# Kernel optimization log

Measured on AMD Instinct MI355X. Metric: run time of the kernel, lower is better.

Reference implementation:

```python
import jax, jax.numpy as jnp
import numpy as np

N_NODES = 100000
N_FEAT = 128
HID = 8
HEADS1 = 8
OUT2 = 32
NEG_SLOPE = 0.2


def gat_conv(x, W, a_src, a_dst, b, src, dst, n_nodes, concat):
    # x: [N, Fin], W: [Fin, H*C], a_src/a_dst: [H, C], b: [H*C] or [C]
    H, C = a_src.shape
    h = (x @ W).reshape(n_nodes, H, C)                      # [N, H, C]
    e_src = jnp.sum(h * a_src, axis=-1)                     # [N, H]
    e_dst = jnp.sum(h * a_dst, axis=-1)                     # [N, H]
    e = jax.nn.leaky_relu(e_src[src] + e_dst[dst], NEG_SLOPE)  # [E, H]
    m = jax.ops.segment_max(e, dst, num_segments=n_nodes)   # [N, H] (self-loops => no empty segment)
    ex = jnp.exp(e - m[dst])                                # [E, H]
    denom = jax.ops.segment_sum(ex, dst, num_segments=n_nodes)
    alpha = ex / denom[dst]                                 # [E, H]
    out = jax.ops.segment_sum(alpha[:, :, None] * h[src], dst, num_segments=n_nodes)  # [N, H, C]
    out = out.reshape(n_nodes, H * C) if concat else out.mean(axis=1)
    return out + b


def setup_inputs() -> dict:
    key = jax.random.key(0)
    ks = jax.random.split(key, 12)
    x = jax.random.normal(ks[0], (N_NODES, N_FEAT), dtype=jnp.float32)
    edge_index = jax.random.randint(ks[1], (2, 3200000), 0, N_NODES, dtype=jnp.int64)
    s1 = 1.0 / np.sqrt(N_FEAT)
    s2 = 1.0 / np.sqrt(HID * HEADS1)
    return {
        "x": x,
        "edge_index": edge_index,
        "W1": jax.random.normal(ks[2], (N_FEAT, HEADS1 * HID), dtype=jnp.float32) * s1,
        "a_src1": jax.random.normal(ks[3], (HEADS1, HID), dtype=jnp.float32) * s2,
        "a_dst1": jax.random.normal(ks[4], (HEADS1, HID), dtype=jnp.float32) * s2,
        "b1": jnp.zeros((HEADS1 * HID,), dtype=jnp.float32),
        "W2": jax.random.normal(ks[5], (HEADS1 * HID, OUT2), dtype=jnp.float32) * s2,
        "a_src2": jax.random.normal(ks[6], (1, OUT2), dtype=jnp.float32) * (1.0 / np.sqrt(OUT2)),
        "a_dst2": jax.random.normal(ks[7], (1, OUT2), dtype=jnp.float32) * (1.0 / np.sqrt(OUT2)),
        "b2": jnp.zeros((OUT2,), dtype=jnp.float32),
        "Wr": jax.random.normal(ks[8], (OUT2, 1), dtype=jnp.float32) * (1.0 / np.sqrt(OUT2)),
        "br": jnp.zeros((1,), dtype=jnp.float32),
    }


def reference(x, edge_index, W1, a_src1, a_dst1, b1, W2, a_src2, a_dst2, b2, Wr, br):
    n = x.shape[0]
    # PyG GATConv default add_self_loops=True
    loops = jnp.arange(n, dtype=edge_index.dtype)
    src = jnp.concatenate([edge_index[0], loops])
    dst = jnp.concatenate([edge_index[1], loops])
    h = gat_conv(x, W1, a_src1, a_dst1, b1, src, dst, n, concat=True)   # [N, 64]
    h = jax.nn.elu(h)
    h = gat_conv(h, W2, a_src2, a_dst2, b2, src, dst, n, concat=False)  # [N, 32]
    pooled = jnp.sum(h, axis=0, keepdims=True)                          # SumAggregation -> [1, 32]
    return pooled @ Wr + br                                             # [1, 1]
```

## Files before the change

### kernel.cpp

```cpp
#include <hip/hip_runtime.h>
#include <math.h>

#define NEG_SLOPE 0.2f
#define FIN 128
#define H1 8
#define F1 64
#define F2 32

#define SHIFT 5
#define BW 32
#define CAPL 2048
#define CAP_G 1408
#define NBMAX 4096

#define SB_SHIFT 11
#define NSBMAX 64
#define P_CHUNK 2048
#define BPS 35
#define SBCAP (BPS * P_CHUNK)

typedef unsigned short ushort_t;
typedef unsigned int uint_t;

#define LO16(u) __uint_as_float((u) << 16)
#define HI16(u) __uint_as_float((u) & 0xffff0000u)

#define FOLDQ4(x) { x += __shfl_xor(x, 16, 64); x += __shfl_xor(x, 32, 64); }
#define FOLD64(x) { x += __shfl_xor(x, 1, 64); x += __shfl_xor(x, 2, 64); x += __shfl_xor(x, 4, 64); \
                    x += __shfl_xor(x, 8, 64); x += __shfl_xor(x, 16, 64); x += __shfl_xor(x, 32, 64); }

static __device__ __forceinline__ ushort_t f2bf(float f) {
    uint_t u = __float_as_uint(f);
    u = (u + 0x7FFFu + ((u >> 16) & 1u)) >> 16;
    return (ushort_t)u;
}
static __device__ __forceinline__ uint_t packAB(float e) {
    return (uint_t)f2bf(__expf(e)) | ((uint_t)f2bf(__expf(NEG_SLOPE * e)) << 16);
}

__global__ void gemm1_kernel(const float* __restrict__ x, const float* __restrict__ W1,
                             const float* __restrict__ a_src, const float* __restrict__ a_dst,
                             ushort_t* __restrict__ h1, uint_t* __restrict__ sp,
                             float* __restrict__ ed, int N) {
    __shared__ float xs[16][FIN];
    int tid = threadIdx.x;
    int n0 = blockIdx.x * 16;
    for (int i = tid; i < 16 * FIN; i += 256) {
        int nn = n0 + (i >> 7);
        xs[i >> 7][i & 127] = (nn < N) ? x[(size_t)nn * FIN + (i & 127)] : 0.f;
    }
    __syncthreads();
    int wv = tid >> 6, j = tid & 63;
    int nb = wv << 2;
    float a0 = 0.f, a1 = 0.f, a2 = 0.f, a3 = 0.f;
#pragma unroll 2
    for (int k = 0; k < FIN; k += 4) {
        float w0 = W1[(k + 0) * F1 + j];
        float w1 = W1[(k + 1) * F1 + j];
        float w2 = W1[(k + 2) * F1 + j];
        float w3 = W1[(k + 3) * F1 + j];
        float4 x0 = *(const float4*)&xs[nb + 0][k];
        float4 x1 = *(const float4*)&xs[nb + 1][k];
        float4 x2 = *(const float4*)&xs[nb + 2][k];
        float4 x3 = *(const float4*)&xs[nb + 3][k];
        a0 = fmaf(x0.x, w0, fmaf(x0.y, w1, fmaf(x0.z, w2, fmaf(x0.w, w3, a0))));
        a1 = fmaf(x1.x, w0, fmaf(x1.y, w1, fmaf(x1.z, w2, fmaf(x1.w, w3, a1))));
        a2 = fmaf(x2.x, w0, fmaf(x2.y, w1, fmaf(x2.z, w2, fmaf(x2.w, w3, a2))));
        a3 = fmaf(x3.x, w0, fmaf(x3.y, w1, fmaf(x3.z, w2, fmaf(x3.w, w3, a3))));
    }
    float as = a_src[j], ad = a_dst[j];
    float av[4] = {a0, a1, a2, a3};
#pragma unroll
    for (int t = 0; t < 4; ++t) {
        int n = n0 + nb + t;
        if (n >= N) break;
        h1[(size_t)n * F1 + j] = f2bf(av[t]);
        float vs = av[t] * as;
        float vd = av[t] * ad;
#pragma unroll
        for (int off = 4; off >= 1; off >>= 1) {
            vs += __shfl_down(vs, off, 8);
            vd += __shfl_down(vd, off, 8);
        }
        if ((j & 7) == 0) {
            sp[n * H1 + (j >> 3)] = packAB(vs);
            ed[n * H1 + (j >> 3)] = vd;
        }
    }
}

__global__ void zerob_kernel(int* __restrict__ bcnt, int* __restrict__ boff,
                             int NB, float* __restrict__ pooled, int capg,
                             int* __restrict__ sbcnt, int nsb,
                             uint_t* __restrict__ sp1, ushort_t* __restrict__ h1, int N) {
    int t = blockIdx.x * blockDim.x + threadIdx.x;
    int stride = gridDim.x * blockDim.x;
    for (int i = t; i < NB; i += stride) {
        bcnt[i] = 0;
        if (capg) boff[i] = i * capg;
    }
    for (int i = t; i < nsb; i += stride) sbcnt[i] = 0;
    if (t < H1) sp1[(size_t)N * H1 + t] = 0u;
    if (t >= 8 && t < 8 + F1) h1[(size_t)N * F1 + (t - 8)] = 0;
    if (t == 72) pooled[0] = 0.f;
}

__global__ void __launch_bounds__(256, 4)
part1_kernel(const int* __restrict__ ei, int E, int N,
             int* __restrict__ sbcnt, uint_t* __restrict__ sbdata) {
    __shared__ int hist[NSBMAX];
    __shared__ int loff[NSBMAX];
    __shared__ int lcur[NSBMAX];
    __shared__ int gb[NSBMAX];
    __shared__ uint_t buf[P_CHUNK];
    __shared__ unsigned char sbarr[P_CHUNK];
    int tid = threadIdx.x;
    int NSB = (N + ((1 << SB_SHIFT) - 1)) >> SB_SHIFT;
    for (int i = tid; i < NSB; i += 256) hist[i] = 0;
    __syncthreads();
    int EN = E + N;
    int base = blockIdx.x * P_CHUNK;
    int m = EN - base; if (m > P_CHUNK) m = P_CHUNK;
    int t0 = base + tid * 8;
    int s[8], d[8];
    bool fast = (t0 + 8 <= E) && ((E & 3) == 0);
    if (fast) {
        int4 a = *(const int4*)&ei[t0];
        int4 b = *(const int4*)&ei[t0 + 4];
        s[0]=a.x; s[1]=a.y; s[2]=a.z; s[3]=a.w; s[4]=b.x; s[5]=b.y; s[6]=b.z; s[7]=b.w;
        int4 c = *(const int4*)&ei[E + t0];
        int4 e2 = *(const int4*)&ei[E + t0 + 4];
        d[0]=c.x; d[1]=c.y; d[2]=c.z; d[3]=c.w; d[4]=e2.x; d[5]=e2.y; d[6]=e2.z; d[7]=e2.w;
    } else {
#pragma unroll
        for (int r = 0; r < 8; ++r) {
            int t = t0 + r;
            if (t < EN) {
                if (t < E) { s[r] = ei[t]; d[r] = ei[E + t]; }
                else       { s[r] = d[r] = t - E; }
            } else d[r] = -1;
        }
    }
#pragma unroll
    for (int r = 0; r < 8; ++r)
        if (d[r] >= 0) atomicAdd(&hist[d[r] >> SB_SHIFT], 1);
    __syncthreads();
    if (tid < 64) {
        int v = (tid < NSB) ? hist[tid] : 0;
        int e = v;
#pragma unroll
        for (int o = 1; o < 64; o <<= 1) {
            int u = __shfl_up(e, o, 64);
            if (tid >= o) e += u;
        }
        e -= v;
        if (tid < NSB) {
            loff[tid] = e;
            lcur[tid] = e;
            gb[tid] = v ? atomicAdd(&sbcnt[tid], v) : 0;
        }
    }
    __syncthreads();
#pragma unroll
    for (int r = 0; r < 8; ++r)
        if (d[r] >= 0) {
            int sb = d[r] >> SB_SHIFT;
            int pos = atomicAdd(&lcur[sb], 1);
            buf[pos] = ((uint_t)s[r] << SB_SHIFT) | (uint_t)(d[r] & ((1 << SB_SHIFT) - 1));
            sbarr[pos] = (unsigned char)sb;
        }
    __syncthreads();
    for (int i = tid; i < m; i += 256) {
        int sb = sbarr[i];
        int idx = gb[sb] + (i - loff[sb]);
        if (idx < SBCAP)
            sbdata[(size_t)sb * SBCAP + idx] = buf[i];
    }
}

__global__ void __launch_bounds__(256, 4)
part2_kernel(const uint_t* __restrict__ sbdata, const int* __restrict__ sbcnt,
             int* __restrict__ bcnt, const int* __restrict__ boff,
             uint_t* __restrict__ pk) {
    __shared__ int hist[64];
    __shared__ int loff[64];
    __shared__ int lcur[64];
    __shared__ int gb[64];
    __shared__ uint_t buf[P_CHUNK];
    int tid = threadIdx.x;
    int sb = blockIdx.x / BPS;
    int base = (blockIdx.x % BPS) * P_CHUNK;
    int cnt = sbcnt[sb];
    if (cnt > SBCAP) cnt = SBCAP;
    if (base >= cnt) return;
    int m = cnt - base; if (m > P_CHUNK) m = P_CHUNK;
    if (tid < 64) hist[tid] = 0;
    __syncthreads();
    const uint_t* src = sbdata + (size_t)sb * SBCAP + base;
    uint_t v[8];
#pragma unroll
    for (int r = 0; r < 8; ++r) {
        int i = tid + r * 256;
        if (i < m) {
            v[r] = src[i];
            atomicAdd(&hist[(v[r] >> 5) & 63], 1);
        }
    }
    __syncthreads();
    if (tid < 64) {
        int c = hist[tid];
        int e = c;
#pragma unroll
        for (int o = 1; o < 64; o <<= 1) {
            int u = __shfl_up(e, o, 64);
            if (tid >= o) e += u;
        }
        e -= c;
        loff[tid] = e;
        lcur[tid] = e;
        int bucket = (sb << 6) + tid;
        gb[tid] = c ? (boff[bucket] + atomicAdd(&bcnt[bucket], c)) : 0;
    }
    __syncthreads();
#pragma unroll
    for (int r = 0; r < 8; ++r) {
        int i = tid + r * 256;
        if (i < m) {
            int lb = (v[r] >> 5) & 63;
            int pos = atomicAdd(&lcur[lb], 1);
            buf[pos] = v[r];
        }
    }
    __syncthreads();
    for (int i = tid; i < m; i += 256) {
        uint_t u = buf[i];
        int lb = (u >> 5) & 63;
        int idx = gb[lb] + (i - loff[lb]);
        pk[idx] = ((u >> SB_SHIFT) << SHIFT) | (u & (BW - 1));
    }
}

__global__ void bhist_kernel(const int* __restrict__ ei, int E, int N,
                             int* __restrict__ bcnt, int NB) {
    __shared__ int h[NBMAX];
    int tid = threadIdx.x;
    for (int i = tid; i < NB; i += 256) h[i] = 0;
    __syncthreads();
    int EN = E + N;
    int chunk = (EN + gridDim.x - 1) / gridDim.x;
    int e0 = blockIdx.x * chunk;
    int e1 = e0 + chunk; if (e1 > EN) e1 = EN;
    for (int t = e0 + tid; t < e1; t += 256) {
        int d = (t < E) ? ei[E + t] : (t - E);
        atomicAdd(&h[d >> SHIFT], 1);
    }
    __syncthreads();
    for (int i = tid; i < NB; i += 256)
        if (h[i]) atomicAdd(&bcnt[i], h[i]);
}

__global__ void bscan_kernel(const int* __restrict__ bcnt, int NB,
                             int* __restrict__ boff, int* __restrict__ bcur) {
    int lane = threadIdx.x;
    int chunk = (NB + 63) >> 6;
    int lo = lane * chunk;
    int hi = lo + chunk; if (hi > NB) hi = NB;
    int sum = 0;
    for (int i = lo; i < hi; ++i) sum += bcnt[i];
    int e = sum;
#pragma unroll
    for (int o = 1; o < 64; o <<= 1) {
        int v = __shfl_up(e, o, 64);
        if (lane >= o) e += v;
    }
    e -= sum;
    int run = e;
    for (int i = lo; i < hi; ++i) {
        int c = bcnt[i];
        boff[i] = run;
        bcur[i] = run;
        run += c;
    }
}

__global__ void bscat_kernel(const int* __restrict__ ei, int E, int N,
                             int* __restrict__ bcur, uint_t* __restrict__ pk, int NB) {
    __shared__ int lh[NBMAX];
    __shared__ int lc[NBMAX];
    int tid = threadIdx.x;
    for (int i = tid; i < NB; i += 256) lh[i] = 0;
    __syncthreads();
    int EN = E + N;
    int chunk = (EN + gridDim.x - 1) / gridDim.x;
    int e0 = blockIdx.x * chunk;
    int e1 = e0 + chunk; if (e1 > EN) e1 = EN;
    for (int t = e0 + tid; t < e1; t += 256) {
        int d = (t < E) ? ei[E + t] : (t - E);
        atomicAdd(&lh[d >> SHIFT], 1);
    }
    __syncthreads();
    for (int i = tid; i < NB; i += 256) {
        int c = lh[i];
        lc[i] = c ? atomicAdd(&bcur[i], c) : 0;
    }
    __syncthreads();
    for (int t = e0 + tid; t < e1; t += 256) {
        int s, d;
        if (t < E) { s = ei[t]; d = ei[E + t]; } else { s = d = t - E; }
        int pos = atomicAdd(&lc[d >> SHIFT], 1);
        pk[pos] = ((uint_t)s << SHIFT) | (uint_t)(d & (BW - 1));
    }
}

__global__ void __launch_bounds__(256, 8)
edge1_gather(const int* __restrict__ bcnt, const int* __restrict__ boff,
             const uint_t* __restrict__ pk,
             const uint_t* __restrict__ sp, const float* __restrict__ ed,
             const ushort_t* __restrict__ h1, float* __restrict__ o1, int N) {
    int b = blockIdx.x;
    int d0 = b << SHIFT;
    int cnt = bcnt[b];
    int gbase = boff[b];
    int tid = threadIdx.x;
    int wv = tid >> 6;
    int L = tid & 63;
    int q = L >> 4;
    int c4 = (L & 15) << 2;
    int hL = (L & 15) >> 1;
    __shared__ int ldeg[BW], loff[BW], lcur[BW];
    __shared__ int lsrc[CAPL];
    if (cnt <= CAPL) {
        if (tid < BW) ldeg[tid] = 0;
        __syncthreads();
        for (int k = tid; k < cnt; k += 256) atomicAdd(&ldeg[pk[gbase + k] & (BW - 1)], 1);
        __syncthreads();
        if (tid < BW) {
            int v = ldeg[tid];
            int e = v;
#pragma unroll
            for (int o = 1; o < BW; o <<= 1) {
                int u = __shfl_up(e, o, 64);
                if (tid >= o) e += u;
            }
            e -= v;
            loff[tid] = e;
            lcur[tid] = e;
        }
        __syncthreads();
        for (int k = tid; k < cnt; k += 256) {
            uint_t v = pk[gbase + k];
            int pos = atomicAdd(&lcur[v & (BW - 1)], 1);
            lsrc[pos] = (int)(v >> SHIFT);
        }
        __syncthreads();
        for (int ld = wv * 8; ld < wv * 8 + 8; ++ld) {
            int d = d0 + ld;
            if (d >= N) break;
            int st = loff[ld], en = st + ldeg[ld];
            float edv = ed[d * H1 + hL];
            float Ad = __expf(edv), Bd = __expf(NEG_SLOPE * edv);
            float ax = 0.f, ay = 0.f, az = 0.f, aw = 0.f, wsum = 0.f;
            uint_t U0, U1; uint2 V0, V1;
            {
                int i0 = st + q, i1 = st + 4 + q;
                bool ok0 = i0 < en, ok1 = i1 < en;
                int s0 = lsrc[ok0 ? i0 : st];
                int s1 = lsrc[ok1 ? i1 : st];
                uint_t u0 = sp[s0 * H1 + hL];
                uint_t u1 = sp[s1 * H1 + hL];
                V0 = *(const uint2*)(h1 + ((size_t)s0 << 6) + c4);
                V1 = *(const uint2*)(h1 + ((size_t)s1 << 6) + c4);
                U0 = ok0 ? u0 : 0u;
                U1 = ok1 ? u1 : 0u;
            }
            for (int k = st; k < en; k += 8) {
                uint_t N0, N1; uint2 P0, P1;
                {
                    int i0 = k + 8 + q, i1 = k + 12 + q;
                    bool ok0 = i0 < en, ok1 = i1 < en;
                    int s0 = lsrc[ok0 ? i0 : st];
                    int s1 = lsrc[ok1 ? i1 : st];
                    uint_t u0 = sp[s0 * H1 + hL];
                    uint_t u1 = sp[s1 * H1 + hL];
                    P0 = *(const uint2*)(h1 + ((size_t)s0 << 6) + c4);
                    P1 = *(const uint2*)(h1 + ((size_t)s1 << 6) + c4);
                    N0 = ok0 ? u0 : 0u;
                    N1 = ok1 ? u1 : 0u;
                }
                float w0 = fmaxf(LO16(U0) * Ad, HI16(U0) * Bd);
                float w1 = fmaxf(LO16(U1) * Ad, HI16(U1) * Bd);
                ax = fmaf(w0, LO16(V0.x), ax);
                ay = fmaf(w0, HI16(V0.x), ay);
                az = fmaf(w0, LO16(V0.y), az);
                aw = fmaf(w0, HI16(V0.y), aw);
                ax = fmaf(w1, LO16(V1.x), ax);
                ay = fmaf(w1, HI16(V1.x), ay);
                az = fmaf(w1, LO16(V1.y), az);
                aw = fmaf(w1, HI16(V1.y), aw);
                wsum += w0 + w1;
                U0 = N0; U1 = N1; V0 = P0; V1 = P1;
            }
            FOLDQ4(ax); FOLDQ4(ay); FOLDQ4(az); FOLDQ4(aw); FOLDQ4(wsum);
            if (q == 0) {
                float inv = 1.f / wsum;
                float4 r; r.x = ax * inv; r.y = ay * inv; r.z = az * inv; r.w = aw * inv;
                *(float4*)(o1 + (size_t)d * F1 + c4) = r;
            }
        }
    } else {
        for (int ld = wv * 8; ld < wv * 8 + 8; ++ld) {
            int d = d0 + ld;
            if (d >= N) break;
            float edv = ed[d * H1 + hL];
            float Ad = __expf(edv), Bd = __expf(NEG_SLOPE * edv);
            float ax = 0.f, ay = 0.f, az = 0.f, aw = 0.f, wsum = 0.f;
            for (int k0 = 0; k0 < cnt; k0 += 4) {
                int idx = k0 + q;
                bool ok = idx < cnt;
                uint_t v = pk[gbase + (ok ? idx : 0)];
                int s = (int)(v >> SHIFT);
                bool m = ok && ((int)(v & (BW - 1)) == ld);
                uint_t u = sp[(uint_t)s * H1 + hL];
                float w = m ? fmaxf(LO16(u) * Ad, HI16(u) * Bd) : 0.f;
                uint2 hv = *(const uint2*)(h1 + ((size_t)s << 6) + c4);
                ax = fmaf(w, LO16(hv.x), ax);
                ay = fmaf(w, HI16(hv.x), ay);
                az = fmaf(w, LO16(hv.y), az);
                aw = fmaf(w, HI16(hv.y), aw);
                wsum += w;
            }
            FOLDQ4(ax); FOLDQ4(ay); FOLDQ4(az); FOLDQ4(aw); FOLDQ4(wsum);
            if (q == 0) {
                float inv = 1.f / wsum;
                float4 r; r.x = ax * inv; r.y = ay * inv; r.z = az * inv; r.w = aw * inv;
                *(float4*)(o1 + (size_t)d * F1 + c4) = r;
            }
        }
    }
}

__global__ void gemm2_kernel(const float* __restrict__ o1, const float* __restrict__ b1,
                             const float* __restrict__ W2,
                             const float* __restrict__ a_src2, const float* __restrict__ a_dst2,
                             const float* __restrict__ Wr,
                             uint2* __restrict__ rec, float* __restrict__ ed2, int N) {
    if (blockIdx.x == 0 && threadIdx.x == 0) {
        uint2 z; z.x = 0u; z.y = 0u;
        rec[N] = z;
    }
    int half = threadIdx.x >> 5;
    int n = blockIdx.x * 8 + half;
    int j = threadIdx.x & 31;
    __shared__ float a1s[8][F1];
    if (n < N) {
#pragma unroll
        for (int r = 0; r < 2; ++r) {
            int k = r * 32 + j;
            float v = o1[(size_t)n * F1 + k] + b1[k];
            a1s[half][k] = v > 0.f ? v : expm1f(v);
        }
    }
    __syncthreads();
    if (n >= N) return;
    float acc = 0.f;
#pragma unroll
    for (int k = 0; k < F1; ++k) acc = fmaf(a1s[half][k], W2[k * F2 + j], acc);
    float vs = acc * a_src2[j];
    float vd = acc * a_dst2[j];
    float vg = acc * Wr[j];
#pragma unroll
    for (int off = 16; off >= 1; off >>= 1) {
        vs += __shfl_down(vs, off, 32);
        vd += __shfl_down(vd, off, 32);
        vg += __shfl_down(vg, off, 32);
    }
    if (j == 0) {
        uint2 r; r.x = packAB(vs); r.y = __float_as_uint(vg);
        rec[n] = r;
        ed2[n] = vd;
    }
}

__global__ void __launch_bounds__(256, 8)
edge2_gather(const int* __restrict__ bcnt, const int* __restrict__ boff,
             const uint_t* __restrict__ pk,
             const uint2* __restrict__ rec, const float* __restrict__ ed2,
             const float* __restrict__ b2, const float* __restrict__ Wr,
             float* __restrict__ pooled, int N) {
    int b = blockIdx.x;
    int d0 = b << SHIFT;
    int cnt = bcnt[b];
    int gbase = boff[b];
    int tid = threadIdx.x;
    int wv = tid >> 6;
    int L = tid & 63;
    __shared__ int ldeg[BW], loff[BW], ldgp[BW], lcur[BW];
    __shared__ int lsrc[CAPL];
    __shared__ float ls[4];
    float t0 = (L < F2) ? b2[L] * Wr[L] : 0.f;
    FOLD64(t0);
    float b2w = t0;
    float part = 0.f;
    if (cnt <= CAPL - 8 * BW - 16) {
        if (tid < BW) ldeg[tid] = 0;
        __syncthreads();
        for (int k = tid; k < cnt; k += 256) atomicAdd(&ldeg[pk[gbase + k] & (BW - 1)], 1);
        __syncthreads();
        if (tid < BW) {
            int v = ldeg[tid];
            int vp = (v + 7) & ~7;
            int e = vp;
#pragma unroll
            for (int o = 1; o < BW; o <<= 1) {
                int u = __shfl_up(e, o, 64);
                if (tid >= o) e += u;
            }
            e -= vp;
            loff[tid] = e;
            lcur[tid] = e;
            ldgp[tid] = vp;
        }
        __syncthreads();
        int tot = loff[BW - 1] + ldgp[BW - 1];
        for (int k = tid; k < tot + 16; k += 256) lsrc[k] = N;
        __syncthreads();
        for (int k = tid; k < cnt; k += 256) {
            uint_t v = pk[gbase + k];
            int pos = atomicAdd(&lcur[v & (BW - 1)], 1);
            lsrc[pos] = (int)(v >> SHIFT);
        }
        __syncthreads();
        for (int ld = wv * 8; ld < wv * 8 + 8; ++ld) {
            int d = d0 + ld;
            if (d >= N) break;
            int st = loff[ld], en = st + ldgp[ld];
            float edv = ed2[d];
            float Ad = __expf(edv), Bd = __expf(NEG_SLOPE * edv);
            float acc = 0.f, wsm = 0.f;
            for (int k = st; k < en; k += 64) {
                int i = k + L;
                bool ok = i < en;
                int s = lsrc[ok ? i : st];
                uint2 r = rec[s];
                float w = ok ? fmaxf(LO16(r.x) * Ad, HI16(r.x) * Bd) : 0.f;
                acc = fmaf(w, __uint_as_float(r.y), acc);
                wsm += w;
            }
            FOLD64(acc); FOLD64(wsm);
            part += acc / wsm + b2w;
        }
    } else {
        for (int ld = wv * 8; ld < wv * 8 + 8; ++ld) {
            int d = d0 + ld;
            if (d >= N) break;
            float edv = ed2[d];
            float Ad = __expf(edv), Bd = __expf(NEG_SLOPE * edv);
            float acc = 0.f, wsm = 0.f;
            for (int k0 = 0; k0 < cnt; k0 += 64) {
                int i = k0 + L;
                bool ok = i < cnt;
                uint_t v = pk[gbase + (ok ? i : 0)];
                int s = (int)(v >> SHIFT);
                bool mm = ok && ((int)(v & (BW - 1)) == ld);
                uint2 r = rec[s];
                float w = mm ? fmaxf(LO16(r.x) * Ad, HI16(r.x) * Bd) : 0.f;
                acc = fmaf(w, __uint_as_float(r.y), acc);
                wsm += w;
            }
            FOLD64(acc); FOLD64(wsm);
            part += acc / wsm + b2w;
        }
    }
    if (L == 0) ls[wv] = part;
    __syncthreads();
    if (tid == 0) atomicAdd(pooled, ls[0] + ls[1] + ls[2] + ls[3]);
}

__global__ void final_kernel(const float* __restrict__ pooled, const float* __restrict__ br,
                             float* __restrict__ out) {
    if (threadIdx.x == 0 && blockIdx.x == 0) out[0] = pooled[0] + br[0];
}

static inline size_t al128(size_t v) { return (v + 127) & ~(size_t)127; }

extern "C" void kernel_launch(void* const* d_in, const int* in_sizes, int n_in,
                              void* d_out, int out_size, void* d_ws, size_t ws_size,
                              hipStream_t stream) {
    const float* x    = (const float*)d_in[0];
    const int*   ei   = (const int*)d_in[1];
    const float* W1   = (const float*)d_in[2];
    const float* a_s1 = (const float*)d_in[3];
    const float* a_d1 = (const float*)d_in[4];
    const float* b1   = (const float*)d_in[5];
    const float* W2   = (const float*)d_in[6];
    const float* a_s2 = (const float*)d_in[7];
    const float* a_d2 = (const float*)d_in[8];
    const float* b2   = (const float*)d_in[9];
    const float* Wr   = (const float*)d_in[10];
    const float* br   = (const float*)d_in[11];
    float* out = (float*)d_out;

    int N = in_sizes[0] / FIN;
    int E = in_sizes[1] / 2;
    size_t n = (size_t)N;
    int NB = (N + BW - 1) >> SHIFT;
    int NSB = (N + ((1 << SB_SHIFT) - 1)) >> SB_SHIFT;

    char* ws = (char*)d_ws;
    size_t off_o1  = 0;
    size_t off_sp1 = al128(off_o1 + n * 256);
    size_t off_ed1 = al128(off_sp1 + n * 32 + 32);
    size_t off_h1  = al128(off_ed1 + n * 32);
    size_t off_pk  = al128(off_h1 + n * 128 + 128);
    float*    o1   = (float*)(ws + off_o1);
    uint_t*   sp1  = (uint_t*)(ws + off_sp1);
    float*    ed1  = (float*)(ws + off_ed1);
    ushort_t* h1   = (ushort_t*)(ws + off_h1);
    uint_t*   pk   = (uint_t*)(ws + off_pk);
    size_t pk_static = (size_t)NB * CAP_G * 4;
    size_t pk_exact  = (size_t)(E + N) * 4;
    uint_t* sbdata = (uint_t*)ws;
    bool use_static = (NSB <= NSBMAX) &&
                      ((size_t)NSB * SBCAP * 4 <= n * 256) &&
                      (ws_size >= off_pk + pk_static + (size_t)NBMAX * 16 +
                                  (size_t)NSBMAX * 4 + 128);
    char* tail = ws + off_pk + (use_static ? pk_static : pk_exact);
    int*      bcnt  = (int*)tail;
    int*      boff  = (int*)(tail + NBMAX * 4);
    int*      bcur  = (int*)(tail + NBMAX * 8);
    int*      sbcnt = (int*)(tail + NBMAX * 12);
    float*  pooled  = (float*)(tail + NBMAX * 12 + NSBMAX * 4);
    uint2* rec = (uint2*)h1;
    float* ed2 = ed1;

    zerob_kernel<<<8, 256, 0, stream>>>(bcnt, boff, NB, pooled,
                                        use_static ? CAP_G : 0, sbcnt, NSB,
                                        sp1, h1, N);
    if (use_static) {
        int EN = E + N;
        int G1 = (EN + P_CHUNK - 1) / P_CHUNK;
        part1_kernel<<<G1, 256, 0, stream>>>(ei, E, N, sbcnt, sbdata);
        part2_kernel<<<NSB * BPS, 256, 0, stream>>>(sbdata, sbcnt, bcnt, boff, pk);
        gemm1_kernel<<<(N + 15) / 16, 256, 0, stream>>>(x, W1, a_s1, a_d1, h1, sp1, ed1, N);
    } else {
        gemm1_kernel<<<(N + 15) / 16, 256, 0, stream>>>(x, W1, a_s1, a_d1, h1, sp1, ed1, N);
        bhist_kernel<<<256, 256, 0, stream>>>(ei, E, N, bcnt, NB);
        bscan_kernel<<<1, 64, 0, stream>>>(bcnt, NB, boff, bcur);
        bscat_kernel<<<256, 256, 0, stream>>>(ei, E, N, bcur, pk, NB);
    }
    edge1_gather<<<NB, 256, 0, stream>>>(bcnt, boff, pk, sp1, ed1, h1, o1, N);
    gemm2_kernel<<<(N + 7) / 8, 256, 0, stream>>>(o1, b1, W2, a_s2, a_d2, Wr, rec, ed2, N);
    edge2_gather<<<NB, 256, 0, stream>>>(bcnt, boff, pk, rec, ed2, b2, Wr, pooled, N);
    final_kernel<<<1, 64, 0, stream>>>(pooled, br, out);
}
```

Measured before the change: 374.3 us.

## Fuse layer-2 GEMM into edge1 gather and reuse its sorted edge lists

The layer-1 aggregation now keeps each block's 32 output rows in shared memory. It applies bias and ELU there, then computes the layer-2 projection and attention scalars in the same kernel, so gemm2 and the o1 round trip through global memory go away. Edge1 also writes the per-destination sorted source list back into pk, together with per-node offsets and degrees. Edge2 then reads those directly instead of rebuilding the local sort with atomics. The cost is extra shared memory in edge1, which may lower occupancy, and edge2 now reads source indices from global memory rather than LDS.

New measurement: 372.7 us (median of 3 runs). About the same (-0.4%).

```diff
diff --git a/kernel.cpp b/kernel.cpp
--- a/kernel.cpp
+++ b/kernel.cpp
@@ -91,8 +91,7 @@
 
 __global__ void zerob_kernel(int* __restrict__ bcnt, int* __restrict__ boff,
                              int NB, float* __restrict__ pooled, int capg,
-                             int* __restrict__ sbcnt, int nsb,
-                             uint_t* __restrict__ sp1, ushort_t* __restrict__ h1, int N) {
+                             int* __restrict__ sbcnt, int nsb) {
     int t = blockIdx.x * blockDim.x + threadIdx.x;
     int stride = gridDim.x * blockDim.x;
     for (int i = t; i < NB; i += stride) {
@@ -100,9 +99,7 @@
         if (capg) boff[i] = i * capg;
     }
     for (int i = t; i < nsb; i += stride) sbcnt[i] = 0;
-    if (t < H1) sp1[(size_t)N * H1 + t] = 0u;
-    if (t >= 8 && t < 8 + F1) h1[(size_t)N * F1 + (t - 8)] = 0;
-    if (t == 72) pooled[0] = 0.f;
+    if (t == 0) pooled[0] = 0.f;
 }
 
 __global__ void __launch_bounds__(256, 4)
@@ -313,10 +310,15 @@
 }
 
 __global__ void __launch_bounds__(256, 8)
-edge1_gather(const int* __restrict__ bcnt, const int* __restrict__ boff,
-             const uint_t* __restrict__ pk,
-             const uint_t* __restrict__ sp, const float* __restrict__ ed,
-             const ushort_t* __restrict__ h1, float* __restrict__ o1, int N) {
+edge1_fused(const int* __restrict__ bcnt, const int* __restrict__ boff,
+            uint_t* __restrict__ pk,
+            const uint_t* __restrict__ sp, const float* __restrict__ ed,
+            const ushort_t* __restrict__ h1,
+            const float* __restrict__ b1, const float* __restrict__ W2,
+            const float* __restrict__ a_src2, const float* __restrict__ a_dst2,
+            const float* __restrict__ Wr,
+            uint2* __restrict__ rec, float* __restrict__ ed2,
+            int* __restrict__ loffg, int* __restrict__ ldegg, int N) {
     int b = blockIdx.x;
     int d0 = b << SHIFT;
     int cnt = bcnt[b];
@@ -329,6 +331,7 @@
     int hL = (L & 15) >> 1;
     __shared__ int ldeg[BW], loff[BW], lcur[BW];
     __shared__ int lsrc[CAPL];
+    __shared__ float a1s[BW][F1];
     if (cnt <= CAPL) {
         if (tid < BW) ldeg[tid] = 0;
         __syncthreads();
@@ -353,6 +356,11 @@
             lsrc[pos] = (int)(v >> SHIFT);
         }
         __syncthreads();
+        for (int k = tid; k < cnt; k += 256) pk[gbase + k] = (uint_t)lsrc[k];
+        if (tid < BW) {
+            loffg[d0 + tid] = loff[tid];
+            ldegg[d0 + tid] = ldeg[tid];
+        }
         for (int ld = wv * 8; ld < wv * 8 + 8; ++ld) {
             int d = d0 + ld;
             if (d >= N) break;
@@ -403,8 +411,10 @@
             FOLDQ4(ax); FOLDQ4(ay); FOLDQ4(az); FOLDQ4(aw); FOLDQ4(wsum);
             if (q == 0) {
                 float inv = 1.f / wsum;
-                float4 r; r.x = ax * inv; r.y = ay * inv; r.z = az * inv; r.w = aw * inv;
-                *(float4*)(o1 + (size_t)d * F1 + c4) = r;
+                a1s[ld][c4 + 0] = ax * inv;
+                a1s[ld][c4 + 1] = ay * inv;
+                a1s[ld][c4 + 2] = az * inv;
+                a1s[ld][c4 + 3] = aw * inv;
             }
         }
     } else {
@@ -432,58 +442,55 @@
             FOLDQ4(ax); FOLDQ4(ay); FOLDQ4(az); FOLDQ4(aw); FOLDQ4(wsum);
             if (q == 0) {
                 float inv = 1.f / wsum;
-                float4 r; r.x = ax * inv; r.y = ay * inv; r.z = az * inv; r.w = aw * inv;
-                *(float4*)(o1 + (size_t)d * F1 + c4) = r;
-            }
-        }
-    }
-}
-
-__global__ void gemm2_kernel(const float* __restrict__ o1, const float* __restrict__ b1,
-                             const float* __restrict__ W2,
-                             const float* __restrict__ a_src2, const float* __restrict__ a_dst2,
-                             const float* __restrict__ Wr,
-                             uint2* __restrict__ rec, float* __restrict__ ed2, int N) {
-    if (blockIdx.x == 0 && threadIdx.x == 0) {
-        uint2 z; z.x = 0u; z.y = 0u;
-        rec[N] = z;
-    }
-    int half = threadIdx.x >> 5;
-    int n = blockIdx.x * 8 + half;
-    int j = threadIdx.x & 31;
-    __shared__ float a1s[8][F1];
-    if (n < N) {
-#pragma unroll
-        for (int r = 0; r < 2; ++r) {
-            int k = r * 32 + j;
-            float v = o1[(size_t)n * F1 + k] + b1[k];
-            a1s[half][k] = v > 0.f ? v : expm1f(v);
-        }
-    }
-    __syncthreads();
-    if (n >= N) return;
-    float acc = 0.f;
-#pragma unroll
-    for (int k = 0; k < F1; ++k) acc = fmaf(a1s[half][k], W2[k * F2 + j], acc);
-    float vs = acc * a_src2[j];
-    float vd = acc * a_dst2[j];
-    float vg = acc * Wr[j];
-#pragma unroll
-    for (int off = 16; off >= 1; off >>= 1) {
-        vs += __shfl_down(vs, off, 32);
-        vd += __shfl_down(vd, off, 32);
-        vg += __shfl_down(vg, off, 32);
-    }
-    if (j == 0) {
-        uint2 r; r.x = packAB(vs); r.y = __float_as_uint(vg);
-        rec[n] = r;
-        ed2[n] = vd;
+                a1s[ld][c4 + 0] = ax * inv;
+                a1s[ld][c4 + 1] = ay * inv;
+                a1s[ld][c4 + 2] = az * inv;
+                a1s[ld][c4 + 3] = aw * inv;
+            }
+        }
+    }
+    int nd = N - d0; if (nd > BW) nd = BW;
+    __syncthreads();
+    for (int i = tid; i < BW * F1; i += 256) {
+        int dd = i >> 6;
+        if (dd < nd) {
+            int k = i & 63;
+            float v = a1s[dd][k] + b1[k];
+            a1s[dd][k] = v > 0.f ? v : expm1f(v);
+        }
+    }
+    __syncthreads();
+    int half = tid >> 5, j = tid & 31;
+#pragma unroll
+    for (int pass = 0; pass < 4; ++pass) {
+        int ld2 = half + (pass << 3);
+        if (ld2 < nd) {
+            float acc = 0.f;
+#pragma unroll
+            for (int k = 0; k < F1; ++k) acc = fmaf(a1s[ld2][k], W2[k * F2 + j], acc);
+            float vs = acc * a_src2[j];
+            float vd = acc * a_dst2[j];
+            float vg = acc * Wr[j];
+#pragma unroll
+            for (int off = 16; off >= 1; off >>= 1) {
+                vs += __shfl_down(vs, off, 32);
+                vd += __shfl_down(vd, off, 32);
+                vg += __shfl_down(vg, off, 32);
+            }
+            if (j == 0) {
+                int d = d0 + ld2;
+                uint2 r; r.x = packAB(vs); r.y = __float_as_uint(vg);
+                rec[d] = r;
+                ed2[d] = vd;
+            }
+        }
     }
 }
 
 __global__ void __launch_bounds__(256, 8)
 edge2_gather(const int* __restrict__ bcnt, const int* __restrict__ boff,
              const uint_t* __restrict__ pk,
+             const int* __restrict__ loffg, const int* __restrict__ ldegg,
              const uint2* __restrict__ rec, const float* __restrict__ ed2,
              const float* __restrict__ b2, const float* __restrict__ Wr,
              float* __restrict__ pooled, int N) {
@@ -494,53 +501,24 @@
     int tid = threadIdx.x;
     int wv = tid >> 6;
     int L = tid & 63;
-    __shared__ int ldeg[BW], loff[BW], ldgp[BW], lcur[BW];
-    __shared__ int lsrc[CAPL];
     __shared__ float ls[4];
     float t0 = (L < F2) ? b2[L] * Wr[L] : 0.f;
     FOLD64(t0);
     float b2w = t0;
     float part = 0.f;
-    if (cnt <= CAPL - 8 * BW - 16) {
-        if (tid < BW) ldeg[tid] = 0;
-        __syncthreads();
-        for (int k = tid; k < cnt; k += 256) atomicAdd(&ldeg[pk[gbase + k] & (BW - 1)], 1);
-        __syncthreads();
-        if (tid < BW) {
-            int v = ldeg[tid];
-            int vp = (v + 7) & ~7;
-            int e = vp;
-#pragma unroll
-            for (int o = 1; o < BW; o <<= 1) {
-                int u = __shfl_up(e, o, 64);
-                if (tid >= o) e += u;
-            }
-            e -= vp;
-            loff[tid] = e;
-            lcur[tid] = e;
-            ldgp[tid] = vp;
-        }
-        __syncthreads();
-        int tot = loff[BW - 1] + ldgp[BW - 1];
-        for (int k = tid; k < tot + 16; k += 256) lsrc[k] = N;
-        __syncthreads();
-        for (int k = tid; k < cnt; k += 256) {
-            uint_t v = pk[gbase + k];
-            int pos = atomicAdd(&lcur[v & (BW - 1)], 1);
-            lsrc[pos] = (int)(v >> SHIFT);
-        }
-        __syncthreads();
+    if (cnt <= CAPL) {
         for (int ld = wv * 8; ld < wv * 8 + 8; ++ld) {
             int d = d0 + ld;
             if (d >= N) break;
-            int st = loff[ld], en = st + ldgp[ld];
+            int st = gbase + loffg[d];
+            int dg = ldegg[d];
             float edv = ed2[d];
             float Ad = __expf(edv), Bd = __expf(NEG_SLOPE * edv);
             float acc = 0.f, wsm = 0.f;
-            for (int k = st; k < en; k += 64) {
+            for (int k = 0; k < dg; k += 64) {
                 int i = k + L;
-                bool ok = i < en;
-                int s = lsrc[ok ? i : st];
+                bool ok = i < dg;
+                int s = (int)pk[st + (ok ? i : 0)];
                 uint2 r = rec[s];
                 float w = ok ? fmaxf(LO16(r.x) * Ad, HI16(r.x) * Bd) : 0.f;
                 acc = fmaf(w, __uint_as_float(r.y), acc);
@@ -607,21 +585,29 @@
     int NSB = (N + ((1 << SB_SHIFT) - 1)) >> SB_SHIFT;
 
     char* ws = (char*)d_ws;
-    size_t off_o1  = 0;
-    size_t off_sp1 = al128(off_o1 + n * 256);
+    size_t off_scr = 0;
+    size_t off_sp1 = al128(off_scr + n * 256);
     size_t off_ed1 = al128(off_sp1 + n * 32 + 32);
     size_t off_h1  = al128(off_ed1 + n * 32);
     size_t off_pk  = al128(off_h1 + n * 128 + 128);
-    float*    o1   = (float*)(ws + off_o1);
     uint_t*   sp1  = (uint_t*)(ws + off_sp1);
     float*    ed1  = (float*)(ws + off_ed1);
     ushort_t* h1   = (ushort_t*)(ws + off_h1);
     uint_t*   pk   = (uint_t*)(ws + off_pk);
     size_t pk_static = (size_t)NB * CAP_G * 4;
     size_t pk_exact  = (size_t)(E + N) * 4;
-    uint_t* sbdata = (uint_t*)ws;
+    uint_t* sbdata = (uint_t*)(ws + off_scr);
+    size_t off_rec  = off_scr;
+    size_t off_ed2  = al128(off_rec + (size_t)NB * BW * 8);
+    size_t off_lofg = al128(off_ed2 + (size_t)NB * BW * 4);
+    size_t off_ldgg = al128(off_lofg + (size_t)NB * BW * 4);
+    uint2* rec   = (uint2*)(ws + off_rec);
+    float* ed2   = (float*)(ws + off_ed2);
+    int*   loffg = (int*)(ws + off_lofg);
+    int*   ldegg = (int*)(ws + off_ldgg);
     bool use_static = (NSB <= NSBMAX) &&
                       ((size_t)NSB * SBCAP * 4 <= n * 256) &&
+                      (off_ldgg + (size_t)NB * BW * 4 <= n * 256) &&
                       (ws_size >= off_pk + pk_static + (size_t)NBMAX * 16 +
                                   (size_t)NSBMAX * 4 + 128);
     char* tail = ws + off_pk + (use_static ? pk_static : pk_exact);
@@ -630,12 +616,9 @@
     int*      bcur  = (int*)(tail + NBMAX * 8);
     int*      sbcnt = (int*)(tail + NBMAX * 12);
     float*  pooled  = (float*)(tail + NBMAX * 12 + NSBMAX * 4);
-    uint2* rec = (uint2*)h1;
-    float* ed2 = ed1;
 
     zerob_kernel<<<8, 256, 0, stream>>>(bcnt, boff, NB, pooled,
-                                        use_static ? CAP_G : 0, sbcnt, NSB,
-                                        sp1, h1, N);
+                                        use_static ? CAP_G : 0, sbcnt, NSB);
     if (use_static) {
         int EN = E + N;
         int G1 = (EN + P_CHUNK - 1) / P_CHUNK;
@@ -648,8 +631,10 @@
         bscan_kernel<<<1, 64, 0, stream>>>(bcnt, NB, boff, bcur);
         bscat_kernel<<<256, 256, 0, stream>>>(ei, E, N, bcur, pk, NB);
     }
-    edge1_gather<<<NB, 256, 0, stream>>>(bcnt, boff, pk, sp1, ed1, h1, o1, N);
-    gemm2_kernel<<<(N + 7) / 8, 256, 0, stream>>>(o1, b1, W2, a_s2, a_d2, Wr, rec, ed2, N);
-    edge2_gather<<<NB, 256, 0, stream>>>(bcnt, boff, pk, rec, ed2, b2, Wr, pooled, N);
+    edge1_fused<<<NB, 256, 0, stream>>>(bcnt, boff, pk, sp1, ed1, h1,
+                                        b1, W2, a_s2, a_d2, Wr,
+                                        rec, ed2, loffg, ldegg, N);
+    edge2_gather<<<NB, 256, 0, stream>>>(bcnt, boff, pk, loffg, ldegg,
+                                         rec, ed2, b2, Wr, pooled, N);
     final_kernel<<<1, 64, 0, stream>>>(pooled, br, out);
 }
```
